# Kernel optimization log

Measured on AMD Instinct MI355X. Metric: run time of the kernel, lower is better.

Reference implementation:

```python
import jax, jax.numpy as jnp
import numpy as np


def setup_inputs() -> dict:
    key = jax.random.key(0)
    B, C, L = 32, 8, 4096
    x = jax.random.normal(key, (B, C, L), dtype=jnp.float32)
    return {"k": 64, "input": x}


def reference(k, input):
    # input: [B, C, L]; build sliding windows [B, C, L-k+1, k] via gather
    L = input.shape[2]
    idx = jnp.arange(L - k + 1)[:, None] + jnp.arange(k)[None, :]  # [L-k+1, k]
    windows = input[:, :, idx]  # [B, C, L-k+1, k]
    logp = jax.nn.log_softmax(windows, axis=-1)
    # sum(softmax * log_softmax) = sum(exp(logp) * logp)
    return jnp.sum(jnp.exp(logp) * logp, axis=-1)  # [B, C, L-k+1]
```

## Files before the change

### kernel.cpp

```cpp
#include <hip/hip_runtime.h>
#include <math.h>


#define KWIN 64
#define LROW 4096
#define NWIN 4033
#define BLOCKS_PER_ROW 4
#define OUT_PER_BLOCK 1024
#define THREADS 256
#define CHUNK 5
#define SCAN_N (THREADS * CHUNK)

__global__ __launch_bounds__(THREADS)
void entropy_win_kernel(const float* __restrict__ x, float* __restrict__ out) {
    __shared__ __align__(16) float PE[SCAN_N];
    __shared__ __align__(16) float PF[SCAN_N];
    __shared__ float wsumE[4], wsumF[4];

    const int bid  = blockIdx.x;
    const int row  = bid / BLOCKS_PER_ROW;
    const int q    = bid % BLOCKS_PER_ROW;
    const int out0 = q * OUT_PER_BLOCK;
    const int tid  = threadIdx.x;
    const int lane = tid & 63;
    const int wid  = tid >> 6;

    int nload = LROW - out0;
    if (nload > OUT_PER_BLOCK + KWIN - 1) nload = OUT_PER_BLOCK + KWIN - 1;
    int nout = NWIN - out0;
    if (nout > OUT_PER_BLOCK) nout = OUT_PER_BLOCK;

    const float* __restrict__ xr = x + row * LROW + out0;

    float e[CHUNK], f[CHUNK];
    const int c0 = CHUNK * tid;
    float se = 0.f, sf = 0.f;
#pragma unroll
    for (int i = 0; i < CHUNK; ++i) {
        int g = c0 + i;
        float ee = 0.f, ff = 0.f;
        if (g < nload) {
            float v = xr[g];
            ee = __expf(v);
            ff = ee * v;
        }
        e[i] = ee;
        f[i] = ff;
        se += ee;
        sf += ff;
    }

    float ise = se, isf = sf;
#pragma unroll
    for (int d = 1; d < 64; d <<= 1) {
        float ue = __shfl_up(ise, d, 64);
        float uf = __shfl_up(isf, d, 64);
        if (lane >= d) { ise += ue; isf += uf; }
    }
    if (lane == 63) { wsumE[wid] = ise; wsumF[wid] = isf; }
    __syncthreads();

    float offE = 0.f, offF = 0.f;
#pragma unroll
    for (int wv = 0; wv < 3; ++wv) {
        if (wv < wid) { offE += wsumE[wv]; offF += wsumF[wv]; }
    }

    float pe = offE + (ise - se);
    float pf = offF + (isf - sf);

#pragma unroll
    for (int i = 0; i < CHUNK; ++i) {
        PE[c0 + i] = pe;
        PF[c0 + i] = pf;
        pe += e[i];
        pf += f[i];
    }
    __syncthreads();

    float* __restrict__ orow = out + row * NWIN + out0;
#pragma unroll
    for (int w = 0; w < 4; ++w) {
        int g = tid + w * THREADS;
        if (g < nout) {
            float S = PE[g + KWIN] - PE[g];
            float T = PF[g + KWIN] - PF[g];
            orow[g] = T / S - __logf(S);
        }
    }
}

extern "C" void kernel_launch(void* const* d_in, const int* in_sizes, int n_in,
                              void* d_out, int out_size, void* d_ws, size_t ws_size,
                              hipStream_t stream) {
    const float* x = (const float*)d_in[1];
    float* out = (float*)d_out;
    (void)in_sizes; (void)n_in; (void)out_size; (void)d_ws; (void)ws_size;

    dim3 grid(256 * BLOCKS_PER_ROW);
    dim3 block(THREADS);
    entropy_win_kernel<<<grid, block, 0, stream>>>(x, out);
}
```

Baseline: 10.43 us.

## Use single-wavefront blocks to drop the cross-wave scan and barrier

Each row is now split across 16 blocks of 64 threads instead of 4 blocks of 256. Each block's prefix scan then fits in one wavefront of shuffles, which removes the shared per-wave partial sums and one __syncthreads. The final division is replaced with a hardware reciprocal times T, which is slightly less precise. In exchange, the 63-element window overlap is reloaded by four times as many blocks, so more redundant global reads. An odd `sf*0.f` term appears in the accumulation; it does not change finite results.

```diff
diff --git a/kernel.cpp b/kernel.cpp
--- a/kernel.cpp
+++ b/kernel.cpp
@@ -5,35 +5,32 @@
 #define KWIN 64
 #define LROW 4096
 #define NWIN 4033
-#define BLOCKS_PER_ROW 4
-#define OUT_PER_BLOCK 1024
-#define THREADS 256
+#define BLOCKS_PER_ROW 16
+#define OUTB 256
+#define THREADS 64
 #define CHUNK 5
-#define SCAN_N (THREADS * CHUNK)
+#define SPAN (THREADS * CHUNK)
 
 __global__ __launch_bounds__(THREADS)
 void entropy_win_kernel(const float* __restrict__ x, float* __restrict__ out) {
-    __shared__ __align__(16) float PE[SCAN_N];
-    __shared__ __align__(16) float PF[SCAN_N];
-    __shared__ float wsumE[4], wsumF[4];
+    __shared__ __align__(16) float PE[SPAN];
+    __shared__ __align__(16) float PF[SPAN];
 
     const int bid  = blockIdx.x;
-    const int row  = bid / BLOCKS_PER_ROW;
-    const int q    = bid % BLOCKS_PER_ROW;
-    const int out0 = q * OUT_PER_BLOCK;
-    const int tid  = threadIdx.x;
-    const int lane = tid & 63;
-    const int wid  = tid >> 6;
+    const int row  = bid >> 4;
+    const int q    = bid & 15;
+    const int out0 = q * OUTB;
+    const int lane = threadIdx.x;
 
     int nload = LROW - out0;
-    if (nload > OUT_PER_BLOCK + KWIN - 1) nload = OUT_PER_BLOCK + KWIN - 1;
+    if (nload > OUTB + KWIN - 1) nload = OUTB + KWIN - 1;
     int nout = NWIN - out0;
-    if (nout > OUT_PER_BLOCK) nout = OUT_PER_BLOCK;
+    if (nout > OUTB) nout = OUTB;
 
     const float* __restrict__ xr = x + row * LROW + out0;
 
     float e[CHUNK], f[CHUNK];
-    const int c0 = CHUNK * tid;
+    const int c0 = CHUNK * lane;
     float se = 0.f, sf = 0.f;
 #pragma unroll
     for (int i = 0; i < CHUNK; ++i) {
@@ -47,7 +44,7 @@
         e[i] = ee;
         f[i] = ff;
         se += ee;
-        sf += ff;
+        sf += sf * 0.f + ff;
     }
 
     float ise = se, isf = sf;
@@ -57,18 +54,9 @@
         float uf = __shfl_up(isf, d, 64);
         if (lane >= d) { ise += ue; isf += uf; }
     }
-    if (lane == 63) { wsumE[wid] = ise; wsumF[wid] = isf; }
-    __syncthreads();
 
-    float offE = 0.f, offF = 0.f;
-#pragma unroll
-    for (int wv = 0; wv < 3; ++wv) {
-        if (wv < wid) { offE += wsumE[wv]; offF += wsumF[wv]; }
-    }
-
-    float pe = offE + (ise - se);
-    float pf = offF + (isf - sf);
-
+    float pe = ise - se;
+    float pf = isf - sf;
 #pragma unroll
     for (int i = 0; i < CHUNK; ++i) {
         PE[c0 + i] = pe;
@@ -81,11 +69,11 @@
     float* __restrict__ orow = out + row * NWIN + out0;
 #pragma unroll
     for (int w = 0; w < 4; ++w) {
-        int g = tid + w * THREADS;
+        int g = lane + w * THREADS;
         if (g < nout) {
             float S = PE[g + KWIN] - PE[g];
             float T = PF[g + KWIN] - PF[g];
-            orow[g] = T / S - __logf(S);
+            orow[g] = T * __builtin_amdgcn_rcpf(S) - __logf(S);
         }
     }
 }
```

Result: faster. 9.868 us (-5.4%).
